# Optimization experiments

Hardware: AMD Instinct MI355X
Metric: run time of the kernel (lower is better)

## Reference

```python
import jax, jax.numpy as jnp
import numpy as np
import math

B, C, L_SEQ, PRED = 32, 21, 512, 96
D, H, DFF, NLAYERS = 512, 8, 2048, 3
E = D // H
PATCH_LEN, STRIDE, PAD = 16, 8, 8
PATCH_NUM = (L_SEQ - PATCH_LEN) // STRIDE + 2  # 64
MA = 25          # moving-average kernel of series_decomp
FACTOR = 1
TOP_K = int(FACTOR * math.log(PATCH_NUM))  # top-k delays in AutoCorrelation


def _pos_embedding(max_len, d_model):
    pos = np.arange(max_len, dtype=np.float32)[:, None]
    div = np.exp(np.arange(0, d_model, 2, dtype=np.float32) * -(math.log(10000.0) / d_model))
    pe = np.zeros((max_len, d_model), np.float32)
    pe[:, 0::2] = np.sin(pos * div)
    pe[:, 1::2] = np.cos(pos * div)
    return jnp.asarray(pe)

POS_EMB = _pos_embedding(PATCH_NUM, D)


def setup_inputs():
    key = jax.random.key(0)
    ks = iter(jax.random.split(key, 48))
    g = lambda shape, s=0.02: jax.random.normal(next(ks), shape, jnp.float32) * s
    inp = {"x_enc": jax.random.normal(next(ks), (B, L_SEQ, C), jnp.float32)}
    inp["w_val"] = g((PATCH_LEN, D))  # PatchEmbedding value_embedding (no bias)
    for tag in ("ac", "sa"):
        for nm in ("Wq", "Wk", "Wv", "Wo"):
            inp[nm + "_" + tag] = g((NLAYERS, D, D))
        for nm in ("bq", "bk", "bv", "bo"):
            inp[nm + "_" + tag] = g((NLAYERS, D))
    inp["Wf"] = g((NLAYERS, 2 * D, D))
    inp["bf"] = g((NLAYERS, D))
    inp["W1"] = g((NLAYERS, D, DFF))   # conv1 (1x1, no bias)
    inp["W2"] = g((NLAYERS, DFF, D))   # conv2 (1x1, no bias)
    inp["bn_g"] = jnp.ones((D,), jnp.float32)
    inp["bn_b"] = jnp.zeros((D,), jnp.float32)
    inp["W_head"] = g((D * PATCH_NUM, PRED))
    inp["b_head"] = g((PRED,))
    return inp


def _proj_heads(x, W, b):
    N, L, _ = x.shape
    return (x @ W + b).reshape(N, L, H, E)


def _auto_corr(x, Wq, bq, Wk, bk, Wv, bv, Wo, bo):
    # AutoCorrelation (training-mode time_delay_agg): FFT correlation + top-k roll aggregation
    N, L, _ = x.shape
    q = _proj_heads(x, Wq, bq)
    k = _proj_heads(x, Wk, bk)
    v = _proj_heads(x, Wv, bv)
    qf = jnp.fft.rfft(q.transpose(0, 2, 3, 1), axis=-1)   # [N,H,E,Lf]
    kf = jnp.fft.rfft(k.transpose(0, 2, 3, 1), axis=-1)
    corr = jnp.fft.irfft(qf * jnp.conj(kf), n=L, axis=-1)  # [N,H,E,L]
    vals = v.transpose(0, 2, 3, 1)                          # [N,H,E,L]
    mean_corr = corr.mean(axis=(1, 2))                      # [N,L]
    _, top_idx = jax.lax.top_k(mean_corr.mean(axis=0), TOP_K)  # delays shared across batch
    w = jax.nn.softmax(mean_corr[:, top_idx], axis=-1)      # [N,TOP_K]
    rolled = jax.vmap(lambda s: jnp.roll(vals, -s, axis=-1))(top_idx)  # [K,N,H,E,L]
    agg = jnp.einsum('knhel,nk->nhel', rolled, w)
    return agg.transpose(0, 3, 1, 2).reshape(N, L, D) @ Wo + bo


def _full_attn(x, Wq, bq, Wk, bk, Wv, bv, Wo, bo):
    N, L, _ = x.shape
    q = _proj_heads(x, Wq, bq)
    k = _proj_heads(x, Wk, bk)
    v = _proj_heads(x, Wv, bv)
    scores = jnp.einsum('blhe,bshe->bhls', q, k) / math.sqrt(E)
    out = jnp.einsum('bhls,bshe->blhe', jax.nn.softmax(scores, axis=-1), v)
    return out.reshape(N, L, D) @ Wo + bo


def _decomp(x):
    # series_decomp: residual after edge-replicated moving average (returns seasonal part)
    half = (MA - 1) // 2
    xp = jnp.concatenate([jnp.repeat(x[:, :1], half, axis=1), x,
                          jnp.repeat(x[:, -1:], half, axis=1)], axis=1)
    cs = jnp.cumsum(xp, axis=1)
    cs = jnp.concatenate([jnp.zeros_like(cs[:, :1]), cs], axis=1)
    mean = (cs[:, MA:] - cs[:, :-MA]) / MA
    return x - mean


def _forward(x_enc, w_val, Wq_ac, bq_ac, Wk_ac, bk_ac, Wv_ac, bv_ac, Wo_ac, bo_ac,
             Wq_sa, bq_sa, Wk_sa, bk_sa, Wv_sa, bv_sa, Wo_sa, bo_sa,
             Wf, bf, W1, W2, bn_g, bn_b, W_head, b_head):
    # instance normalization over time
    means = x_enc.mean(axis=1, keepdims=True)                 # [B,1,C]
    xc = x_enc - means
    stdev = jnp.sqrt(xc.var(axis=1, keepdims=True) + 1e-5)    # [B,1,C]
    xn = xc / stdev
    # patch embedding (channel independent): replication-pad end, unfold, linear + pos emb
    xp = xn.transpose(0, 2, 1)                                # [B,C,L]
    xp = jnp.concatenate([xp, jnp.repeat(xp[..., -1:], PAD, axis=-1)], axis=-1)
    idx = jnp.arange(PATCH_NUM)[:, None] * STRIDE + jnp.arange(PATCH_LEN)[None, :]
    patches = xp[..., idx]                                    # [B,C,P,patch_len]
    x = patches.reshape(B * C, PATCH_NUM, PATCH_LEN) @ w_val + POS_EMB  # [B*C,P,D]
    # hybrid encoder layers
    for l in range(NLAYERS):
        a = _auto_corr(x, Wq_ac[l], bq_ac[l], Wk_ac[l], bk_ac[l], Wv_ac[l], bv_ac[l], Wo_ac[l], bo_ac[l])
        s = _full_attn(x, Wq_sa[l], bq_sa[l], Wk_sa[l], bk_sa[l], Wv_sa[l], bv_sa[l], Wo_sa[l], bo_sa[l])
        fused = jnp.concatenate([a, s], axis=-1) @ Wf[l] + bf[l]
        x = _decomp(x + fused)
        y = jax.nn.relu(x @ W1[l]) @ W2[l]                    # 1x1 convs == pointwise linears
        x = _decomp(x + y)
    # final BatchNorm1d over d_model channels (batch statistics, affine)
    mu = x.mean(axis=(0, 1))
    var = x.var(axis=(0, 1))
    x = (x - mu) / jnp.sqrt(var + 1e-5) * bn_g + bn_b
    # head: [B*C,P,D] -> [B,C,D,P] -> flat (d-major) -> pred_len
    enc = x.reshape(B, C, PATCH_NUM, D).transpose(0, 1, 3, 2).reshape(B, C, D * PATCH_NUM)
    dec = (enc @ W_head + b_head).transpose(0, 2, 1)          # [B,PRED,C]
    return dec * stdev[:, 0][:, None, :] + means[:, 0][:, None, :]


def reference(x_enc, w_val, Wq_ac, bq_ac, Wk_ac, bk_ac, Wv_ac, bv_ac, Wo_ac, bo_ac,
              Wq_sa, bq_sa, Wk_sa, bk_sa, Wv_sa, bv_sa, Wo_sa, bo_sa,
              Wf, bf, W1, W2, bn_g, bn_b, W_head, b_head):
    return _forward(x_enc, w_val, Wq_ac, bq_ac, Wk_ac, bk_ac, Wv_ac, bv_ac, Wo_ac, bo_ac,
                    Wq_sa, bq_sa, Wk_sa, bk_sa, Wv_sa, bv_sa, Wo_sa, bo_sa,
                    Wf, bf, W1, W2, bn_g, bn_b, W_head, b_head)
```

## Files before the change

kernel.cpp:

```cpp
#include <hip/hip_runtime.h>
#include <math.h>


typedef unsigned short u16;
typedef short s16x8 __attribute__((ext_vector_type(8)));
typedef u16 u16x8 __attribute__((ext_vector_type(8)));
typedef float f32x4 __attribute__((ext_vector_type(4)));

#define MROWS 43008
#define NSEQ  672

__device__ __forceinline__ float bf2f(u16 b) {
  union { unsigned u; float f; } v; v.u = ((unsigned)b) << 16; return v.f;
}
__device__ __forceinline__ u16 f2bf(float f) {
  union { float f; unsigned u; } v; v.f = f;
  unsigned r = v.u + 0x7FFFu + ((v.u >> 16) & 1u);
  return (u16)(r >> 16);
}

__device__ __forceinline__ void gload16(const u16* g, u16* l) {
  __builtin_amdgcn_global_load_lds(
      (const __attribute__((address_space(1))) unsigned int*)g,
      (__attribute__((address_space(3))) unsigned int*)l, 16, 0, 0);
}

__global__ __launch_bounds__(256) void zero_out_kernel(float* __restrict__ o, int n) {
  int i = blockIdx.x * 256 + threadIdx.x;
  if (i < n) o[i] = 0.f;
}

__global__ __launch_bounds__(256) void transpose_cvt_b(
    const float* __restrict__ W, u16* __restrict__ Wt, int K, int N,
    long long sW, long long sT) {
  __shared__ float t[32][33];
  int z = blockIdx.z;
  W += (size_t)z * sW;
  Wt += (size_t)z * sT;
  int k0 = blockIdx.x * 32, n0 = blockIdx.y * 32;
  int tx = threadIdx.x, ty = threadIdx.y;
#pragma unroll
  for (int i = 0; i < 32; i += 8)
    t[ty + i][tx] = W[(size_t)(k0 + ty + i) * N + n0 + tx];
  __syncthreads();
#pragma unroll
  for (int i = 0; i < 32; i += 8)
    Wt[(size_t)(n0 + ty + i) * K + k0 + tx] = f2bf(t[tx][ty + i]);
}

__global__ __launch_bounds__(256) void transpose_cvt_sa(
    const float* __restrict__ Wq_sa, const float* __restrict__ Wk_sa,
    const float* __restrict__ Wv_sa, u16* __restrict__ dst) {
  __shared__ float t[32][33];
  int z = blockIdx.z;
  int l = z / 3, wi = z % 3;
  const float* srcs[3] = {Wq_sa, Wk_sa, Wv_sa};
  const float* W = srcs[wi] + (size_t)l * 262144;
  u16* out = dst + ((size_t)l * 3 + wi) * 262144;
  int k0 = blockIdx.x * 32, n0 = blockIdx.y * 32;
  int tx = threadIdx.x, ty = threadIdx.y;
#pragma unroll
  for (int i = 0; i < 32; i += 8)
    t[ty + i][tx] = W[(size_t)(k0 + ty + i) * 512 + n0 + tx];
  __syncthreads();
#pragma unroll
  for (int i = 0; i < 32; i += 8)
    out[(size_t)(n0 + ty + i) * 512 + k0 + tx] = f2bf(t[tx][ty + i]);
}

__global__ __launch_bounds__(256) void cvt_bf16_fifteen(
    const float* __restrict__ Wo_ac, const float* __restrict__ Wo_sa,
    const float* __restrict__ Wv_ac, const float* __restrict__ Wq_ac,
    const float* __restrict__ Wk_ac, u16* __restrict__ dst) {
  int z = blockIdx.z;
  int l = z / 5, s = z % 5;
  const float* bases[5] = {Wo_ac, Wo_sa, Wv_ac, Wq_ac, Wk_ac};
  const float* src = bases[s] + (size_t)l * 262144;
  u16* out = dst + ((size_t)l * 5 + s) * 262144;
  int i = blockIdx.x * 256 + threadIdx.x;
  if (i < 262144) out[i] = f2bf(src[i]);
}

__global__ __launch_bounds__(512) void boa_eff_kernel(
    const float* __restrict__ Wo_ac, const float* __restrict__ bo_ac,
    const float* __restrict__ bv_ac, float* __restrict__ out) {
  int l = blockIdx.x;
  int i = threadIdx.x;
  const float* Wo = Wo_ac + (size_t)l * 262144;
  float s = bo_ac[l * 512 + i];
  for (int k = 0; k < 512; k++) s += bv_ac[l * 512 + k] * Wo[(size_t)k * 512 + i];
  out[l * 512 + i] = s;
}

__global__ __launch_bounds__(512) void bias_combine(
    const float* __restrict__ WfW, const float* __restrict__ bfW,
    const float* __restrict__ boa_eff, const float* __restrict__ bo_sa,
    float* __restrict__ out) {
  int l = blockIdx.x;
  const float* Wf = WfW + (size_t)l * 524288;
  int n = threadIdx.x;
  float s = bfW[l * 512 + n];
  for (int i = 0; i < 512; i++) s += boa_eff[l * 512 + i] * Wf[(size_t)i * 512 + n];
  for (int i = 0; i < 512; i++) s += bo_sa[l * 512 + i] * Wf[(size_t)(512 + i) * 512 + n];
  out[l * 512 + n] = s;
}

__global__ __launch_bounds__(512, 4) void gemm128x256(
    const u16* __restrict__ A1, const u16* __restrict__ A2, int lda, int ksplit,
    const u16* __restrict__ Bt, int ldb,
    const float* __restrict__ b0, const float* __restrict__ b1,
    const float* __restrict__ b2,
    u16* __restrict__ C, int ldc, int K, int relu, int nb) {
  __shared__ u16 smA[3][128 * 32];
  __shared__ u16 smB[3][256 * 32];
  int g = blockIdx.x;
  if ((gridDim.x & 7) == 0) g = (g & 7) * (gridDim.x >> 3) + (g >> 3);
  int m0 = (g / nb) * 128, n0 = (g % nb) * 256;
  int tid = threadIdx.x, lane = tid & 63, wid = tid >> 6;
  int wr = wid >> 2, wc = wid & 3;
  int m_in = lane & 15, kq = lane >> 4;
  int sr = tid >> 2;
  int gsl = (((tid & 3) ^ ((sr >> 1) & 3)) * 8);

  int offA[4], offB[4];
#pragma unroll
  for (int mf = 0; mf < 4; mf++) {
    int row = wr * 64 + mf * 16 + m_in;
    offA[mf] = row * 32 + ((kq ^ ((row >> 1) & 3)) * 8);
  }
#pragma unroll
  for (int nf = 0; nf < 4; nf++) {
    int row = wc * 64 + nf * 16 + m_in;
    offB[nf] = row * 32 + ((kq ^ ((row >> 1) & 3)) * 8);
  }
  f32x4 acc[4][4];
#pragma unroll
  for (int i = 0; i < 4; i++)
#pragma unroll
    for (int j = 0; j < 4; j++) acc[i][j] = (f32x4){0.f, 0.f, 0.f, 0.f};

  int nt = K >> 5;
  auto STAGE = [&](int b, int t) {
    int k0 = t * 32;
    const u16* Ap; int kk;
    if (k0 < ksplit) { Ap = A1; kk = k0; } else { Ap = A2; kk = k0 - ksplit; }
    gload16(&Ap[(size_t)(m0 + sr) * lda + kk + gsl], &smA[b][wid * 512]);
    gload16(&Bt[(size_t)(n0 + sr) * ldb + k0 + gsl], &smB[b][wid * 512]);
    gload16(&Bt[(size_t)(n0 + 128 + sr) * ldb + k0 + gsl],
            &smB[b][4096 + wid * 512]);
  };

  STAGE(0, 0);
  STAGE(1, 1 < nt ? 1 : nt - 1);
  int cb = 0;
  for (int t = 0; t < nt; ++t) {
    int pf = t + 2 < nt ? t + 2 : nt - 1;
    int pb = cb + 2 >= 3 ? cb - 1 : cb + 2;
    STAGE(pb, pf);
    asm volatile("s_waitcnt vmcnt(6)" ::: "memory");
    asm volatile("s_barrier" ::: "memory");
    const u16* la = &smA[cb][0];
    const u16* lb = &smB[cb][0];
    s16x8 a_[4], b_[4];
#pragma unroll
    for (int mf = 0; mf < 4; mf++) a_[mf] = *(const s16x8*)&la[offA[mf]];
#pragma unroll
    for (int nf = 0; nf < 4; nf++) b_[nf] = *(const s16x8*)&lb[offB[nf]];
    __builtin_amdgcn_s_setprio(1);
#pragma unroll
    for (int mf = 0; mf < 4; mf++)
#pragma unroll
      for (int nf = 0; nf < 4; nf++)
        acc[mf][nf] = __builtin_amdgcn_mfma_f32_16x16x32_bf16(
            a_[mf], b_[nf], acc[mf][nf], 0, 0, 0);
    __builtin_amdgcn_s_setprio(0);
    asm volatile("s_barrier" ::: "memory");
    cb = cb + 1 >= 3 ? 0 : cb + 1;
  }
  int r0 = m0 + wr * 64 + (kq << 2);
#pragma unroll
  for (int mf = 0; mf < 4; mf++) {
#pragma unroll
    for (int nf = 0; nf < 4; nf++) {
      int col = n0 + wc * 64 + nf * 16 + m_in;
      const float* bp = (col < 512) ? b0 : (col < 1024 ? b1 : b2);
      float bv = bp ? bp[col & 511] : 0.f;
#pragma unroll
      for (int r = 0; r < 4; r++) {
        float v = acc[mf][nf][r] + bv;
        if (relu) v = fmaxf(v, 0.f);
        C[(size_t)(r0 + mf * 16 + r) * ldc + col] = f2bf(v);
      }
    }
  }
}

__global__ __launch_bounds__(256) void gemm128p(
    const u16* __restrict__ A1, const u16* __restrict__ A2, int lda, int ksplit,
    const u16* __restrict__ Bt, int ldb,
    const float* __restrict__ b0, const float* __restrict__ b1,
    const float* __restrict__ b2,
    u16* __restrict__ C, int ldc, int K, int relu, int nb,
    long long syA, long long syB, long long syC) {
  __shared__ u16 sm[3][8192];
  int zy = blockIdx.y;
  A1 += (size_t)zy * syA;
  A2 += (size_t)zy * syA;
  Bt += (size_t)zy * syB;
  C  += (size_t)zy * syC;
  int g = blockIdx.x;
  if ((gridDim.x & 7) == 0) g = (g & 7) * (gridDim.x >> 3) + (g >> 3);
  int m0 = (g / nb) * 128, n0 = (g % nb) * 128;
  int tid = threadIdx.x, lane = tid & 63, w = tid >> 6;
  int wr = w >> 1, wc = w & 1;
  int srow = w * 16 + (lane >> 2);
  int scol = (((lane & 3) ^ ((lane >> 3) & 3)) * 8);
  int m_in = lane & 15;
  int sgrp = lane >> 4;
  int offA[4], offB[4];
#pragma unroll
  for (int mf = 0; mf < 4; mf++) {
    int row = wr * 64 + mf * 16 + m_in;
    offA[mf] = row * 32 + ((sgrp ^ ((row >> 1) & 3)) * 8);
  }
#pragma unroll
  for (int nf = 0; nf < 4; nf++) {
    int row = wc * 64 + nf * 16 + m_in;
    offB[nf] = 4096 + row * 32 + ((sgrp ^ ((row >> 1) & 3)) * 8);
  }
  f32x4 acc[4][4];
#pragma unroll
  for (int i = 0; i < 4; i++)
#pragma unroll
    for (int j = 0; j < 4; j++) acc[i][j] = (f32x4){0.f, 0.f, 0.f, 0.f};

  int nt = K >> 5;
  auto STAGE = [&](int b, int t) {
    int k0 = t * 32;
    const u16* Ab; int kk;
    if (k0 < ksplit) { Ab = A1; kk = k0; } else { Ab = A2; kk = k0 - ksplit; }
    u16* base = &sm[b][0];
    gload16(&Ab[(size_t)(m0 + srow) * lda + kk + scol],      base + w * 512);
    gload16(&Ab[(size_t)(m0 + 64 + srow) * lda + kk + scol], base + 2048 + w * 512);
    gload16(&Bt[(size_t)(n0 + srow) * ldb + k0 + scol],      base + 4096 + w * 512);
    gload16(&Bt[(size_t)(n0 + 64 + srow) * ldb + k0 + scol], base + 6144 + w * 512);
  };

  STAGE(0, 0);
  STAGE(1, 1 < nt ? 1 : nt - 1);
  int cb = 0;
  for (int t = 0; t < nt; ++t) {
    int pf = t + 2 < nt ? t + 2 : nt - 1;
    int pb = cb + 2 >= 3 ? cb - 1 : cb + 2;
    STAGE(pb, pf);
    asm volatile("s_waitcnt vmcnt(8)" ::: "memory");
    asm volatile("s_barrier" ::: "memory");
    const u16* lb = &sm[cb][0];
    s16x8 a_[4], b_[4];
#pragma unroll
    for (int mf = 0; mf < 4; mf++) a_[mf] = *(const s16x8*)&lb[offA[mf]];
#pragma unroll
    for (int nf = 0; nf < 4; nf++) b_[nf] = *(const s16x8*)&lb[offB[nf]];
    __builtin_amdgcn_s_setprio(1);
#pragma unroll
    for (int mf = 0; mf < 4; mf++)
#pragma unroll
      for (int nf = 0; nf < 4; nf++)
        acc[mf][nf] = __builtin_amdgcn_mfma_f32_16x16x32_bf16(
            a_[mf], b_[nf], acc[mf][nf], 0, 0, 0);
    __builtin_amdgcn_s_setprio(0);
    asm volatile("s_barrier" ::: "memory");
    cb = cb + 1 >= 3 ? 0 : cb + 1;
  }
  int r0 = m0 + wr * 64 + (sgrp << 2);
  int cl = lane & 15;
#pragma unroll
  for (int mf = 0; mf < 4; mf++) {
#pragma unroll
    for (int nf = 0; nf < 4; nf++) {
      int col = n0 + wc * 64 + nf * 16 + cl;
      const float* bp = (col < 512) ? b0 : (col < 1024 ? b1 : b2);
      float bv = bp ? bp[col & 511] : 0.f;
#pragma unroll
      for (int r = 0; r < 4; r++) {
        float v = acc[mf][nf][r] + bv;
        if (relu) v = fmaxf(v, 0.f);
        C[(size_t)(r0 + mf * 16 + r) * ldc + col] = f2bf(v);
      }
    }
  }
}

__global__ __launch_bounds__(256) void gram_mc_kernel(
    const u16* __restrict__ Q, int ldq, const u16* __restrict__ K, int ldk,
    float* __restrict__ MC) {
  __shared__ u16 lA[64][40];
  __shared__ u16 lB[64][40];
  __shared__ float red[64];
  int n = blockIdx.x;
  int tid = threadIdx.x, lane = tid & 63, w = tid >> 6;
  int sr = tid >> 2, scol = (tid & 3) * 8;
  if (tid < 64) red[tid] = 0.f;
  f32x4 acc[4];
#pragma unroll
  for (int i = 0; i < 4; i++) acc[i] = (f32x4){0.f, 0.f, 0.f, 0.f};
  size_t bq = (size_t)n * 64 * ldq;
  size_t bk = (size_t)n * 64 * ldk;
  for (int k0 = 0; k0 < 512; k0 += 32) {
    *(u16x8*)&lA[sr][scol] = *(const u16x8*)&Q[bq + (size_t)sr * ldq + k0 + scol];
    *(u16x8*)&lB[sr][scol] = *(const u16x8*)&K[bk + (size_t)sr * ldk + k0 + scol];
    __syncthreads();
    int ar = w * 16 + (lane & 15);
    int kk = (lane >> 4) * 8;
    s16x8 af = *(const s16x8*)&lA[ar][kk];
#pragma unroll
    for (int nb = 0; nb < 4; nb++) {
      s16x8 bfr = *(const s16x8*)&lB[nb * 16 + (lane & 15)][kk];
      acc[nb] = __builtin_amdgcn_mfma_f32_16x16x32_bf16(af, bfr, acc[nb], 0, 0, 0);
    }
    __syncthreads();
  }
  int row0 = w * 16 + ((lane >> 4) << 2);
  int cl = lane & 15;
#pragma unroll
  for (int nb = 0; nb < 4; nb++) {
    int col = nb * 16 + cl;
#pragma unroll
    for (int r = 0; r < 4; r++)
      atomicAdd(&red[(row0 + r - col) & 63], acc[nb][r]);
  }
  __syncthreads();
  if (tid < 64) MC[n * 64 + tid] = red[tid] * (1.f / 512.f);
}

__global__ __launch_bounds__(256) void instnorm_kernel(
    const float* __restrict__ xe, float* __restrict__ MEANS, float* __restrict__ STDEV) {
  int n = blockIdx.x;
  int b = n / 21, c = n % 21;
  int tid = threadIdx.x;
  float v0 = xe[((size_t)b * 512 + tid) * 21 + c];
  float v1 = xe[((size_t)b * 512 + tid + 256) * 21 + c];
  float s = v0 + v1, ss = v0 * v0 + v1 * v1;
  for (int o = 32; o; o >>= 1) { s += __shfl_down(s, o); ss += __shfl_down(ss, o); }
  __shared__ float rs[4], rss[4];
  if ((tid & 63) == 0) { rs[tid >> 6] = s; rss[tid >> 6] = ss; }
  __syncthreads();
  if (tid == 0) {
    s = rs[0] + rs[1] + rs[2] + rs[3];
    ss = rss[0] + rss[1] + rss[2] + rss[3];
    float mean = s * (1.f / 512.f);
    float var = ss * (1.f / 512.f) - mean * mean;
    MEANS[n] = mean;
    STDEV[n] = sqrtf(var + 1e-5f);
  }
}

__global__ __launch_bounds__(256) void pe_kernel(float* __restrict__ PE) {
  int i = blockIdx.x * 256 + threadIdx.x;
  int p = i >> 9, d = i & 511;
  int k = d >> 1;
  float freq = expf(-(float)(2 * k) * (9.210340371976184f / 512.f));
  float ang = (float)p * freq;
  PE[i] = (d & 1) ? cosf(ang) : sinf(ang);
}

__global__ __launch_bounds__(256) void patch_kernel(
    const float* __restrict__ xe, const float* __restrict__ wv,
    const float* __restrict__ PE, const float* __restrict__ MEANS,
    const float* __restrict__ STDEV, u16* __restrict__ X) {
  __shared__ float pw[16][512];
  __shared__ float pat[8][16];
  int bx = blockIdx.x;
  int n = bx >> 3, pb = bx & 7;
  int b = n / 21, c = n % 21;
  int tid = threadIdx.x;
  float mean = MEANS[n], inv = 1.f / STDEV[n];
  for (int i = tid; i < 8192; i += 256) pw[i >> 9][i & 511] = wv[i];
  if (tid < 128) {
    int pp = tid >> 4, j = tid & 15;
    int l = (pb * 8 + pp) * 8 + j;
    if (l > 511) l = 511;
    pat[pp][j] = (xe[((size_t)b * 512 + l) * 21 + c] - mean) * inv;
  }
  __syncthreads();
  for (int i = tid; i < 4096; i += 256) {
    int pp = i >> 9, d = i & 511;
    int p = pb * 8 + pp;
    float s = PE[p * 512 + d];
#pragma unroll
    for (int j = 0; j < 16; j++) s += pat[pp][j] * pw[j][d];
    X[((size_t)n * 64 + p) * 512 + d] = f2bf(s);
  }
}

__global__ __launch_bounds__(256) void topk_softw_kernel(
    const float* __restrict__ MC, int* __restrict__ TIDX, float* __restrict__ WSM) {
  __shared__ float g[256];
  __shared__ float gt[64];
  __shared__ int dly[4];
  int tid = threadIdx.x;
  int tau = tid & 63, part = tid >> 6;
  float s = 0.f;
  for (int n = part * 168; n < (part + 1) * 168; n++) s += MC[n * 64 + tau];
  g[tid] = s;
  __syncthreads();
  if (tid < 64) gt[tid] = g[tid] + g[64 + tid] + g[128 + tid] + g[192 + tid];
  __syncthreads();
  if (tid == 0) {
    for (int j = 0; j < 4; j++) {
      int best = 0; float bv = -1e30f;
      for (int t = 0; t < 64; t++) if (gt[t] > bv) { bv = gt[t]; best = t; }
      dly[j] = best;
      TIDX[j] = best;
      gt[best] = -1e30f;
    }
  }
  __syncthreads();
  for (int n = tid; n < 672; n += 256) {
    float v[4], mx = -1e30f;
#pragma unroll
    for (int j = 0; j < 4; j++) { v[j] = MC[n * 64 + dly[j]]; mx = fmaxf(mx, v[j]); }
    float ssum = 0.f;
#pragma unroll
    for (int j = 0; j < 4; j++) { v[j] = __expf(v[j] - mx); ssum += v[j]; }
    float inv = 1.f / ssum;
#pragma unroll
    for (int j = 0; j < 4; j++) WSM[n * 4 + j] = v[j] * inv;
  }
}

__global__ __launch_bounds__(256) void agg_kernel(
    const u16* __restrict__ V, int ldv, const float* __restrict__ WSM,
    const int* __restrict__ TIDX, u16* __restrict__ OUT, int ldo) {
  int n = blockIdx.x;
  __shared__ float w[4];
  __shared__ int dly[4];
  int tid = threadIdx.x;
  if (tid < 4) { w[tid] = WSM[n * 4 + tid]; dly[tid] = TIDX[tid]; }
  __syncthreads();
  for (int i = tid; i < 64 * 512; i += 256) {
    int l = i >> 9, d = i & 511;
    float s = 0.f;
#pragma unroll
    for (int j = 0; j < 4; j++)
      s += w[j] * bf2f(V[((size_t)n * 64 + ((l + dly[j]) & 63)) * ldv + d]);
    OUT[((size_t)n * 64 + l) * ldo + d] = f2bf(s);
  }
}

__global__ __launch_bounds__(256) void attn_mfma(u16* __restrict__ QKV) {
  __shared__ u16 lq[64][72], lk[64][72], lvt[64][72], lp[64][72];
  int n = blockIdx.x >> 3, h = blockIdx.x & 7;
  size_t base = (size_t)n * 64 * 1536;
  int qo = h * 64, ko = 512 + h * 64, vo = 1024 + h * 64;
  int tid = threadIdx.x, lane = tid & 63, w = tid >> 6;
  int r = tid >> 2, c0 = (tid & 3) * 16;
  *(u16x8*)&lq[r][c0]     = *(const u16x8*)&QKV[base + (size_t)r * 1536 + qo + c0];
  *(u16x8*)&lq[r][c0 + 8] = *(const u16x8*)&QKV[base + (size_t)r * 1536 + qo + c0 + 8];
  *(u16x8*)&lk[r][c0]     = *(const u16x8*)&QKV[base + (size_t)r * 1536 + ko + c0];
  *(u16x8*)&lk[r][c0 + 8] = *(const u16x8*)&QKV[base + (size_t)r * 1536 + ko + c0 + 8];
  u16x8 v0 = *(const u16x8*)&QKV[base + (size_t)r * 1536 + vo + c0];
  u16x8 v1 = *(const u16x8*)&QKV[base + (size_t)r * 1536 + vo + c0 + 8];
#pragma unroll
  for (int j = 0; j < 8; j++) { lvt[c0 + j][r] = v0[j]; lvt[c0 + 8 + j][r] = v1[j]; }
  __syncthreads();
  int m_in = lane & 15, ks = (lane >> 4) * 8;
  int rq = lane >> 4;
  s16x8 aq0 = *(const s16x8*)&lq[w * 16 + m_in][ks];
  s16x8 aq1 = *(const s16x8*)&lq[w * 16 + m_in][32 + ks];
  f32x4 s4[4];
#pragma unroll
  for (int nf = 0; nf < 4; nf++) {
    s4[nf] = (f32x4){0.f, 0.f, 0.f, 0.f};
    s16x8 b0 = *(const s16x8*)&lk[nf * 16 + m_in][ks];
    s16x8 b1 = *(const s16x8*)&lk[nf * 16 + m_in][32 + ks];
    s4[nf] = __builtin_amdgcn_mfma_f32_16x16x32_bf16(aq0, b0, s4[nf], 0, 0, 0);
    s4[nf] = __builtin_amdgcn_mfma_f32_16x16x32_bf16(aq1, b1, s4[nf], 0, 0, 0);
  }
  float mx[4] = {-1e30f, -1e30f, -1e30f, -1e30f};
#pragma unroll
  for (int nf = 0; nf < 4; nf++)
#pragma unroll
    for (int r4 = 0; r4 < 4; r4++) {
      s4[nf][r4] *= 0.125f;
      mx[r4] = fmaxf(mx[r4], s4[nf][r4]);
    }
#pragma unroll
  for (int o = 1; o < 16; o <<= 1)
#pragma unroll
    for (int r4 = 0; r4 < 4; r4++) mx[r4] = fmaxf(mx[r4], __shfl_xor(mx[r4], o));
  float sum[4] = {0.f, 0.f, 0.f, 0.f};
#pragma unroll
  for (int nf = 0; nf < 4; nf++)
#pragma unroll
    for (int r4 = 0; r4 < 4; r4++) {
      float e = __expf(s4[nf][r4] - mx[r4]);
      s4[nf][r4] = e;
      sum[r4] += e;
    }
#pragma unroll
  for (int o = 1; o < 16; o <<= 1)
#pragma unroll
    for (int r4 = 0; r4 < 4; r4++) sum[r4] += __shfl_xor(sum[r4], o);
#pragma unroll
  for (int nf = 0; nf < 4; nf++)
#pragma unroll
    for (int r4 = 0; r4 < 4; r4++)
      lp[w * 16 + rq * 4 + r4][nf * 16 + m_in] = f2bf(s4[nf][r4] / sum[r4]);
  __syncthreads();
  s16x8 ap0 = *(const s16x8*)&lp[w * 16 + m_in][ks];
  s16x8 ap1 = *(const s16x8*)&lp[w * 16 + m_in][32 + ks];
#pragma unroll
  for (int nf = 0; nf < 4; nf++) {
    f32x4 o4 = (f32x4){0.f, 0.f, 0.f, 0.f};
    s16x8 b0 = *(const s16x8*)&lvt[nf * 16 + m_in][ks];
    s16x8 b1 = *(const s16x8*)&lvt[nf * 16 + m_in][32 + ks];
    o4 = __builtin_amdgcn_mfma_f32_16x16x32_bf16(ap0, b0, o4, 0, 0, 0);
    o4 = __builtin_amdgcn_mfma_f32_16x16x32_bf16(ap1, b1, o4, 0, 0, 0);
#pragma unroll
    for (int r4 = 0; r4 < 4; r4++)
      QKV[base + (size_t)(w * 16 + rq * 4 + r4) * 1536 + qo + nf * 16 + m_in] =
          f2bf(o4[r4]);
  }
}

__global__ __launch_bounds__(256) void decomp_kernel(
    u16* __restrict__ X, const u16* __restrict__ DELTA, int ds) {
  int n = blockIdx.x >> 1;
  int d = ((blockIdx.x & 1) << 8) + threadIdx.x;
  size_t xb = ((size_t)n * 64) * 512 + d;
  size_t db = ((size_t)n * 64) * ds + d;
  float v[64];
#pragma unroll
  for (int l = 0; l < 64; l++)
    v[l] = bf2f(X[xb + (size_t)l * 512]) + bf2f(DELTA[db + (size_t)l * ds]);
  float s = 12.f * v[0];
#pragma unroll
  for (int t = 0; t <= 12; t++) s += v[t];
#pragma unroll
  for (int l = 0; l < 64; l++) {
    float out = v[l] - s * (1.f / 25.f);
    X[xb + (size_t)l * 512] = f2bf(out);
    if (l < 63) {
      int add = l + 13; if (add > 63) add = 63;
      int sub = l - 12; if (sub < 0) sub = 0;
      s += v[add] - v[sub];
    }
  }
}

__global__ __launch_bounds__(256) void bn_part(
    const u16* __restrict__ X, float* __restrict__ PS) {
  int ch = blockIdx.x, tid = threadIdx.x;
  float s1a = 0, s2a = 0, s1b = 0, s2b = 0;
  size_t base = (size_t)ch * 128 * 512;
  for (int r = 0; r < 128; r++) {
    float a = bf2f(X[base + (size_t)r * 512 + tid]);
    float b = bf2f(X[base + (size_t)r * 512 + tid + 256]);
    s1a += a; s2a += a * a; s1b += b; s2b += b * b;
  }
  PS[(size_t)(ch * 2 + 0) * 512 + tid] = s1a;
  PS[(size_t)(ch * 2 + 0) * 512 + tid + 256] = s1b;
  PS[(size_t)(ch * 2 + 1) * 512 + tid] = s2a;
  PS[(size_t)(ch * 2 + 1) * 512 + tid + 256] = s2b;
}

__global__ __launch_bounds__(256) void bn_final(
    const float* __restrict__ PS, const float* __restrict__ g,
    const float* __restrict__ b, float* __restrict__ SCALE, float* __restrict__ SHIFT) {
  int d = blockIdx.x * 256 + threadIdx.x;
  float s = 0, ss = 0;
  for (int c = 0; c < 336; c++) {
    s += PS[(size_t)(c * 2) * 512 + d];
    ss += PS[(size_t)(c * 2 + 1) * 512 + d];
  }
  float mu = s * (1.f / 43008.f);
  float var = ss * (1.f / 43008.f) - mu * mu;
  float inv = 1.f / sqrtf(var + 1e-5f);
  float sc = g[d] * inv;
  SCALE[d] = sc;
  SHIFT[d] = b[d] - mu * sc;
}

__global__ __launch_bounds__(256) void bn_transpose_kernel(
    const u16* __restrict__ X, const float* __restrict__ SCALE,
    const float* __restrict__ SHIFT, u16* __restrict__ ENC) {
  __shared__ u16 t[64][72];
  int n = blockIdx.x >> 3, dc = (blockIdx.x & 7) * 64;
  int tid = threadIdx.x;
  for (int i = tid; i < 4096; i += 256) {
    int p = i >> 6, d = i & 63;
    float v = bf2f(X[((size_t)n * 64 + p) * 512 + dc + d]) * SCALE[dc + d] + SHIFT[dc + d];
    t[p][d] = f2bf(v);
  }
  __syncthreads();
  for (int i = tid; i < 4096; i += 256) {
    int d = i >> 6, p = i & 63;
    ENC[(size_t)n * 32768 + (size_t)(dc + d) * 64 + p] = t[p][d];
  }
}

__global__ __launch_bounds__(256) void head_gemm(
    const u16* __restrict__ ENC, const u16* __restrict__ Wht,
    float* __restrict__ PART) {
  __shared__ u16 lA[64][40];
  __shared__ u16 lB[96][40];
  int bm = blockIdx.x;
  int kc = blockIdx.y;
  int tid = threadIdx.x, lane = tid & 63, w = tid >> 6;
  int sr = tid >> 2, sc0 = (tid & 3) * 8;
  f32x4 acc[6];
#pragma unroll
  for (int i = 0; i < 6; i++) acc[i] = (f32x4){0.f, 0.f, 0.f, 0.f};
  for (int kk0 = 0; kk0 < 2048; kk0 += 32) {
    int k0 = kc * 2048 + kk0;
    *(u16x8*)&lA[sr][sc0] =
        *(const u16x8*)&ENC[(size_t)(bm * 64 + sr) * 32768 + k0 + sc0];
    for (int i = tid; i < 96 * 4; i += 256) {
      int rB = i >> 2, seg = (i & 3) * 8;
      *(u16x8*)&lB[rB][seg] = *(const u16x8*)&Wht[(size_t)rB * 32768 + k0 + seg];
    }
    __syncthreads();
    int ar = w * 16 + (lane & 15);
    int kk = (lane >> 4) * 8;
    s16x8 af = *(const s16x8*)&lA[ar][kk];
#pragma unroll
    for (int nb = 0; nb < 6; nb++) {
      s16x8 bfr = *(const s16x8*)&lB[nb * 16 + (lane & 15)][kk];
      acc[nb] = __builtin_amdgcn_mfma_f32_16x16x32_bf16(af, bfr, acc[nb], 0, 0, 0);
    }
    __syncthreads();
  }
  int rb = bm * 64 + w * 16 + ((lane >> 4) << 2);
  int cl = lane & 15;
#pragma unroll
  for (int nb = 0; nb < 6; nb++) {
    int col = nb * 16 + cl;
#pragma unroll
    for (int r = 0; r < 4; r++) {
      int row = rb + r;
      if (row < 672) PART[((size_t)kc * 672 + row) * 96 + col] = acc[nb][r];
    }
  }
}

__global__ __launch_bounds__(256) void head_reduce(
    const float* __restrict__ PART, const float* __restrict__ bh,
    const float* __restrict__ STDEV, const float* __restrict__ MEANS,
    float* __restrict__ OUT) {
  int i = blockIdx.x * 256 + threadIdx.x;
  if (i >= 672 * 96) return;
  int n = i / 96, r = i % 96;
  float s = bh[r];
  for (int kc = 0; kc < 16; kc++) s += PART[((size_t)kc * 672 + n) * 96 + r];
  int b = n / 21, c = n % 21;
  OUT[((size_t)b * 96 + r) * 21 + c] = s * STDEV[n] + MEANS[n];
}

extern "C" void kernel_launch(void* const* d_in, const int* in_sizes, int n_in,
                              void* d_out, int out_size, void* d_ws, size_t ws_size,
                              hipStream_t stream) {
  const float* x_enc = (const float*)d_in[0];
  const float* w_val = (const float*)d_in[1];
  const float* Wq_ac = (const float*)d_in[2];
  const float* Wk_ac = (const float*)d_in[3];
  const float* Wv_ac = (const float*)d_in[4];
  const float* Wo_ac = (const float*)d_in[5];
  const float* bq_ac = (const float*)d_in[6];
  const float* bk_ac = (const float*)d_in[7];
  const float* bv_ac = (const float*)d_in[8];
  const float* bo_ac = (const float*)d_in[9];
  const float* Wq_sa = (const float*)d_in[10];
  const float* Wk_sa = (const float*)d_in[11];
  const float* Wv_sa = (const float*)d_in[12];
  const float* Wo_sa = (const float*)d_in[13];
  const float* bq_sa = (const float*)d_in[14];
  const float* bk_sa = (const float*)d_in[15];
  const float* bv_sa = (const float*)d_in[16];
  const float* bo_sa = (const float*)d_in[17];
  const float* WfW   = (const float*)d_in[18];
  const float* bfW   = (const float*)d_in[19];
  const float* W1    = (const float*)d_in[20];
  const float* W2    = (const float*)d_in[21];
  const float* bn_g  = (const float*)d_in[22];
  const float* bn_b  = (const float*)d_in[23];
  const float* W_head = (const float*)d_in[24];
  const float* b_head = (const float*)d_in[25];
  (void)in_sizes; (void)n_in; (void)out_size;
  (void)bq_ac; (void)bk_ac;

  char* wsp = (char*)d_ws;
  size_t off = 0;
  auto alloc = [&](size_t bytes) -> void* {
    void* p = wsp + off;
    off += (bytes + 255) & ~(size_t)255;
    return p;
  };
  u16* X    = (u16*)alloc((size_t)MROWS * 512 * 2);
  u16* Q3   = (u16*)alloc((size_t)MROWS * 1536 * 2);
  u16* SIX   = (u16*)alloc((size_t)3 * 3 * 262144 * 2);
  u16* W1T   = (u16*)alloc((size_t)3 * 1048576 * 2);
  u16* W2T   = (u16*)alloc((size_t)3 * 1048576 * 2);
  u16* WFT   = (u16*)alloc((size_t)3 * 524288 * 2);
  u16* WORIG = (u16*)alloc((size_t)3 * 5 * 262144 * 2);
  u16* WCOMB = (u16*)alloc((size_t)3 * 524288 * 2);
  u16* WQKT  = (u16*)alloc((size_t)3 * 262144 * 2);
  u16* WHT   = (u16*)alloc((size_t)3145728 * 2);
  u16* TMP   = (u16*)alloc((size_t)3 * 262144 * 2);
  float* PE = (float*)alloc((size_t)32768 * 4);
  float* MEANS = (float*)alloc(672 * 4);
  float* STDEV = (float*)alloc(672 * 4);
  float* MC = (float*)alloc(672 * 64 * 4);
  int* TIDX = (int*)alloc(4 * 4);
  float* WSM = (float*)alloc(672 * 4 * 4);
  float* BNP = (float*)alloc((size_t)336 * 1024 * 4);
  float* SCALE = (float*)alloc(512 * 4);
  float* SHIFT = (float*)alloc(512 * 4);
  float* BOAE = (float*)alloc(3 * 512 * 4);
  float* BCOMB = (float*)alloc(3 * 512 * 4);
  u16* C0 = Q3;
  u16* C1 = Q3 + 512;
  u16* C2 = Q3 + 1024;
  u16* HBUF = Q3;
  u16* YBUF = Q3 + (size_t)21504 * 2048;
  u16* ENC  = Q3;
  float* HEADP = (float*)X;

  if (off > ws_size) {
    zero_out_kernel<<<252, 256, 0, stream>>>((float*)d_out, 672 * 96);
    return;
  }

  transpose_cvt_sa<<<dim3(16, 16, 9), dim3(32, 8), 0, stream>>>(
      Wq_sa, Wk_sa, Wv_sa, SIX);
  transpose_cvt_b<<<dim3(16, 64, 3), dim3(32, 8), 0, stream>>>(
      W1, W1T, 512, 2048, 1048576, 1048576);
  transpose_cvt_b<<<dim3(64, 16, 3), dim3(32, 8), 0, stream>>>(
      W2, W2T, 2048, 512, 1048576, 1048576);
  transpose_cvt_b<<<dim3(32, 16, 3), dim3(32, 8), 0, stream>>>(
      WfW, WFT, 1024, 512, 524288, 524288);
  transpose_cvt_b<<<dim3(1024, 3, 1), dim3(32, 8), 0, stream>>>(
      W_head, WHT, 32768, 96, 0, 0);
  cvt_bf16_fifteen<<<dim3(1024, 1, 15), 256, 0, stream>>>(
      Wo_ac, Wo_sa, Wv_ac, Wq_ac, Wk_ac, WORIG);
  boa_eff_kernel<<<3, 512, 0, stream>>>(Wo_ac, bo_ac, bv_ac, BOAE);
  bias_combine<<<3, 512, 0, stream>>>(WfW, bfW, BOAE, bo_sa, BCOMB);
  gemm128p<<<dim3(16, 3), 256, 0, stream>>>(
      WFT, WFT, 1024, 512, WORIG, 512, nullptr, nullptr, nullptr,
      TMP, 512, 512, 0, 4, 524288, 5 * 262144, 262144);
  gemm128p<<<dim3(16, 3), 256, 0, stream>>>(
      TMP, TMP, 512, 512, WORIG + 2 * 262144, 512, nullptr, nullptr, nullptr,
      WCOMB, 1024, 512, 0, 4, 262144, 5 * 262144, 524288);
  gemm128p<<<dim3(16, 3), 256, 0, stream>>>(
      WFT + 512, WFT + 512, 1024, 512, WORIG + 262144, 512,
      nullptr, nullptr, nullptr, WCOMB + 512, 1024, 512, 0, 4,
      524288, 5 * 262144, 524288);
  gemm128p<<<dim3(16, 3), 256, 0, stream>>>(
      WORIG + 4 * 262144, WORIG + 4 * 262144, 512, 512,
      WORIG + 3 * 262144, 512, nullptr, nullptr, nullptr,
      WQKT, 512, 512, 0, 4, 5 * 262144, 5 * 262144, 262144);

  instnorm_kernel<<<672, 256, 0, stream>>>(x_enc, MEANS, STDEV);
  pe_kernel<<<128, 256, 0, stream>>>(PE);
  patch_kernel<<<672 * 8, 256, 0, stream>>>(x_enc, w_val, PE, MEANS, STDEV, X);

  auto gbig = [&](const u16* A1, const u16* A2, int lda, int ksplit,
                  const u16* Bt, int ldb, const float* b0, const float* b1,
                  const float* b2, u16* C, int ldc, int M, int N, int K,
                  int relu) {
    int nb = N / 256;
    if (nb < 1) nb = 1;
    gemm128x256<<<(M / 128) * nb, 512, 0, stream>>>(
        A1, A2, lda, ksplit, Bt, ldb, b0, b1, b2, C, ldc, K, relu, nb);
  };

  for (int l = 0; l < 3; l++) {
    const u16* qkv_sa = SIX + (size_t)l * 3 * 262144;
    const u16* wqkt   = WQKT + (size_t)l * 262144;
    const u16* w1     = W1T + (size_t)l * 1048576;
    const u16* w2     = W2T + (size_t)l * 1048576;
    const u16* wcomb  = WCOMB + (size_t)l * 524288;
    gbig(X, X, 512, 512, qkv_sa, 512, bq_sa + l * 512, bk_sa + l * 512,
         bv_sa + l * 512, Q3, 1536, MROWS, 1536, 512, 0);
    attn_mfma<<<5376, 256, 0, stream>>>(Q3);
    gbig(X, X, 512, 512, wqkt, 512, nullptr, nullptr, nullptr,
         C1, 1536, MROWS, 512, 512, 0);
    gram_mc_kernel<<<672, 256, 0, stream>>>(C1, 1536, X, 512, MC);
    topk_softw_kernel<<<1, 256, 0, stream>>>(MC, TIDX, WSM);
    agg_kernel<<<672, 256, 0, stream>>>(X, 512, WSM, TIDX, C2, 1536);
    gbig(C2, C0, 1536, 512, wcomb, 1024, BCOMB + l * 512, nullptr, nullptr,
         C1, 1536, MROWS, 512, 1024, 0);
    decomp_kernel<<<1344, 256, 0, stream>>>(X, C1, 1536);
    for (int c = 0; c < 2; c++) {
      const u16* Xc = X + (size_t)c * 21504 * 512;
      u16* Yc = YBUF + (size_t)c * 21504 * 512;
      gbig(Xc, Xc, 512, 512, w1, 512, nullptr, nullptr, nullptr,
           HBUF, 2048, 21504, 2048, 512, 1);
      gemm128x256<<<(21504 / 128) * 2, 512, 0, stream>>>(
          HBUF, HBUF, 2048, 2048, w2, 2048, nullptr, nullptr, nullptr,
          Yc, 512, 2048, 0, 2);
    }
    decomp_kernel<<<1344, 256, 0, stream>>>(X, YBUF, 512);
  }

  bn_part<<<336, 256, 0, stream>>>(X, BNP);
  bn_final<<<2, 256, 0, stream>>>(BNP, bn_g, bn_b, SCALE, SHIFT);
  bn_transpose_kernel<<<672 * 8, 256, 0, stream>>>(X, SCALE, SHIFT, ENC);
  head_gemm<<<dim3(11, 16), 256, 0, stream>>>(ENC, WHT, HEADP);
  head_reduce<<<252, 256, 0, stream>>>(HEADP, b_head, STDEV, MEANS, (float*)d_out);
}
```

Baseline: 2.160 ms.

## Enlarge GEMM tile to 256x256 with split-phase loads interleaved with MFMA

Replaces the 128x256 bf16 MFMA GEMM with a 256x256 tile, where each wave computes 128x64 with 8x4 accumulators. The LDS ring grows to four stages. A and B global-to-LDS loads are now issued in two halves, each overlapped with half of the MFMA work. The aim is to raise arithmetic intensity per byte loaded and hide load latency. The cost is double the LDS use (128 KB) and more registers, which limits occupancy to about 2 blocks, and M must be divisible by 256.

```diff
diff --git a/kernel.cpp b/kernel.cpp
--- a/kernel.cpp
+++ b/kernel.cpp
@@ -105,27 +105,25 @@
   out[l * 512 + n] = s;
 }
 
-__global__ __launch_bounds__(512, 4) void gemm128x256(
+__global__ __launch_bounds__(512, 2) void gemm256f(
     const u16* __restrict__ A1, const u16* __restrict__ A2, int lda, int ksplit,
     const u16* __restrict__ Bt, int ldb,
     const float* __restrict__ b0, const float* __restrict__ b1,
     const float* __restrict__ b2,
     u16* __restrict__ C, int ldc, int K, int relu, int nb) {
-  __shared__ u16 smA[3][128 * 32];
-  __shared__ u16 smB[3][256 * 32];
+  __shared__ u16 smA[4][256 * 32];
+  __shared__ u16 smB[4][256 * 32];
   int g = blockIdx.x;
   if ((gridDim.x & 7) == 0) g = (g & 7) * (gridDim.x >> 3) + (g >> 3);
-  int m0 = (g / nb) * 128, n0 = (g % nb) * 256;
+  int m0 = (g / nb) * 256, n0 = (g % nb) * 256;
   int tid = threadIdx.x, lane = tid & 63, wid = tid >> 6;
   int wr = wid >> 2, wc = wid & 3;
   int m_in = lane & 15, kq = lane >> 4;
-  int sr = tid >> 2;
-  int gsl = (((tid & 3) ^ ((sr >> 1) & 3)) * 8);
-
-  int offA[4], offB[4];
-#pragma unroll
-  for (int mf = 0; mf < 4; mf++) {
-    int row = wr * 64 + mf * 16 + m_in;
+
+  int offA[8], offB[4];
+#pragma unroll
+  for (int mf = 0; mf < 8; mf++) {
+    int row = wr * 128 + mf * 16 + m_in;
     offA[mf] = row * 32 + ((kq ^ ((row >> 1) & 3)) * 8);
   }
 #pragma unroll
@@ -133,53 +131,85 @@
     int row = wc * 64 + nf * 16 + m_in;
     offB[nf] = row * 32 + ((kq ^ ((row >> 1) & 3)) * 8);
   }
-  f32x4 acc[4][4];
-#pragma unroll
-  for (int i = 0; i < 4; i++)
+  int srow[2], sgcol[2], sbase[2];
+#pragma unroll
+  for (int l = 0; l < 2; l++) {
+    int idx = l * 512 + tid;
+    int row = idx >> 2, sl = idx & 3;
+    srow[l] = row;
+    sgcol[l] = (sl ^ ((row >> 1) & 3)) * 8;
+    sbase[l] = (l * 512 + wid * 64) * 8;
+  }
+
+  f32x4 acc[8][4];
+#pragma unroll
+  for (int i = 0; i < 8; i++)
 #pragma unroll
     for (int j = 0; j < 4; j++) acc[i][j] = (f32x4){0.f, 0.f, 0.f, 0.f};
 
-  int nt = K >> 5;
-  auto STAGE = [&](int b, int t) {
-    int k0 = t * 32;
+  int nu = K >> 5;
+
+  auto STAGE_A = [&](int ds, int u) {
+    int k0 = u * 32;
     const u16* Ap; int kk;
     if (k0 < ksplit) { Ap = A1; kk = k0; } else { Ap = A2; kk = k0 - ksplit; }
-    gload16(&Ap[(size_t)(m0 + sr) * lda + kk + gsl], &smA[b][wid * 512]);
-    gload16(&Bt[(size_t)(n0 + sr) * ldb + k0 + gsl], &smB[b][wid * 512]);
-    gload16(&Bt[(size_t)(n0 + 128 + sr) * ldb + k0 + gsl],
-            &smB[b][4096 + wid * 512]);
+#pragma unroll
+    for (int l = 0; l < 2; l++)
+      gload16(&Ap[(size_t)(m0 + srow[l]) * lda + kk + sgcol[l]],
+              &smA[ds][sbase[l]]);
   };
-
-  STAGE(0, 0);
-  STAGE(1, 1 < nt ? 1 : nt - 1);
-  int cb = 0;
-  for (int t = 0; t < nt; ++t) {
-    int pf = t + 2 < nt ? t + 2 : nt - 1;
-    int pb = cb + 2 >= 3 ? cb - 1 : cb + 2;
-    STAGE(pb, pf);
-    asm volatile("s_waitcnt vmcnt(6)" ::: "memory");
+  auto STAGE_B = [&](int ds, int u) {
+    int k0 = u * 32;
+#pragma unroll
+    for (int l = 0; l < 2; l++)
+      gload16(&Bt[(size_t)(n0 + srow[l]) * ldb + k0 + sgcol[l]],
+              &smB[ds][sbase[l]]);
+  };
+
+  STAGE_A(0, 0); STAGE_B(0, 0);
+  STAGE_A(1, 1); STAGE_B(1, 1);
+  asm volatile("s_waitcnt vmcnt(4)" ::: "memory");
+  asm volatile("s_barrier" ::: "memory");
+
+  for (int u = 0; u < nu; ++u) {
+    int sl = u & 3, ds = (u + 2) & 3;
+    int usrc = (u + 2 < nu) ? u + 2 : u;
+    const u16* As = &smA[sl][0];
+    const u16* Bs = &smB[sl][0];
+    s16x8 a_[8], b_[4];
+#pragma unroll
+    for (int mf = 0; mf < 8; mf++) a_[mf] = *(const s16x8*)&As[offA[mf]];
+    b_[0] = *(const s16x8*)&Bs[offB[0]];
+    b_[1] = *(const s16x8*)&Bs[offB[1]];
+    STAGE_A(ds, usrc);
     asm volatile("s_barrier" ::: "memory");
-    const u16* la = &smA[cb][0];
-    const u16* lb = &smB[cb][0];
-    s16x8 a_[4], b_[4];
-#pragma unroll
-    for (int mf = 0; mf < 4; mf++) a_[mf] = *(const s16x8*)&la[offA[mf]];
-#pragma unroll
-    for (int nf = 0; nf < 4; nf++) b_[nf] = *(const s16x8*)&lb[offB[nf]];
     __builtin_amdgcn_s_setprio(1);
 #pragma unroll
-    for (int mf = 0; mf < 4; mf++)
-#pragma unroll
-      for (int nf = 0; nf < 4; nf++)
+    for (int mf = 0; mf < 8; mf++)
+#pragma unroll
+      for (int nf = 0; nf < 2; nf++)
         acc[mf][nf] = __builtin_amdgcn_mfma_f32_16x16x32_bf16(
             a_[mf], b_[nf], acc[mf][nf], 0, 0, 0);
     __builtin_amdgcn_s_setprio(0);
     asm volatile("s_barrier" ::: "memory");
-    cb = cb + 1 >= 3 ? 0 : cb + 1;
-  }
-  int r0 = m0 + wr * 64 + (kq << 2);
-#pragma unroll
-  for (int mf = 0; mf < 4; mf++) {
+    b_[2] = *(const s16x8*)&Bs[offB[2]];
+    b_[3] = *(const s16x8*)&Bs[offB[3]];
+    STAGE_B(ds, usrc);
+    asm volatile("s_barrier" ::: "memory");
+    __builtin_amdgcn_s_setprio(1);
+#pragma unroll
+    for (int mf = 0; mf < 8; mf++)
+#pragma unroll
+      for (int nf = 2; nf < 4; nf++)
+        acc[mf][nf] = __builtin_amdgcn_mfma_f32_16x16x32_bf16(
+            a_[mf], b_[nf], acc[mf][nf], 0, 0, 0);
+    __builtin_amdgcn_s_setprio(0);
+    asm volatile("s_waitcnt vmcnt(4)" ::: "memory");
+    asm volatile("s_barrier" ::: "memory");
+  }
+  int r0 = m0 + wr * 128 + (kq << 2);
+#pragma unroll
+  for (int mf = 0; mf < 8; mf++) {
 #pragma unroll
     for (int nf = 0; nf < 4; nf++) {
       int col = n0 + wc * 64 + nf * 16 + m_in;
@@ -770,7 +800,7 @@
                   int relu) {
     int nb = N / 256;
     if (nb < 1) nb = 1;
-    gemm128x256<<<(M / 128) * nb, 512, 0, stream>>>(
+    gemm256f<<<(M / 256) * nb, 512, 0, stream>>>(
         A1, A2, lda, ksplit, Bt, ldb, b0, b1, b2, C, ldc, K, relu, nb);
   };
 
@@ -796,9 +826,8 @@
       u16* Yc = YBUF + (size_t)c * 21504 * 512;
       gbig(Xc, Xc, 512, 512, w1, 512, nullptr, nullptr, nullptr,
            HBUF, 2048, 21504, 2048, 512, 1);
-      gemm128x256<<<(21504 / 128) * 2, 512, 0, stream>>>(
-          HBUF, HBUF, 2048, 2048, w2, 2048, nullptr, nullptr, nullptr,
-          Yc, 512, 2048, 0, 2);
+      gbig(HBUF, HBUF, 2048, 2048, w2, 2048, nullptr, nullptr, nullptr,
+           Yc, 512, 21504, 512, 2048, 0);
     }
     decomp_kernel<<<1344, 256, 0, stream>>>(X, YBUF, 512);
   }
```

Measured after the change: 2.225 ms. 1.03x slower.

## Fuse residual add and series decomposition into GEMM epilogue

Applied to the files above, without the earlier changes.

Adds a decomposition epilogue mode to the 128x256 GEMM. Each wave adds the residual X to its accumulator tile, stages the 64-row tile in shared memory, runs the 25-tap moving-average subtraction along the sequence, and writes the result back into X in place. This removes both decomp_kernel launches per layer, along with the intermediate C1 and YBUF write and read round trips. In exchange the shared arrays are merged into one buffer reused as per-wave scratch, the epilogue does strided column writes, and the kernel relies on each 64-row sequence block sitting inside one wave's tile.

```diff
diff --git a/kernel.cpp b/kernel.cpp
--- a/kernel.cpp
+++ b/kernel.cpp
@@ -110,9 +110,8 @@
     const u16* __restrict__ Bt, int ldb,
     const float* __restrict__ b0, const float* __restrict__ b1,
     const float* __restrict__ b2,
-    u16* __restrict__ C, int ldc, int K, int relu, int nb) {
-  __shared__ u16 smA[3][128 * 32];
-  __shared__ u16 smB[3][256 * 32];
+    u16* __restrict__ C, int ldc, int K, int relu, int nb, int dmode) {
+  __shared__ u16 shm[36864];
   int g = blockIdx.x;
   if ((gridDim.x & 7) == 0) g = (g & 7) * (gridDim.x >> 3) + (g >> 3);
   int m0 = (g / nb) * 128, n0 = (g % nb) * 256;
@@ -144,10 +143,11 @@
     int k0 = t * 32;
     const u16* Ap; int kk;
     if (k0 < ksplit) { Ap = A1; kk = k0; } else { Ap = A2; kk = k0 - ksplit; }
-    gload16(&Ap[(size_t)(m0 + sr) * lda + kk + gsl], &smA[b][wid * 512]);
-    gload16(&Bt[(size_t)(n0 + sr) * ldb + k0 + gsl], &smB[b][wid * 512]);
+    gload16(&Ap[(size_t)(m0 + sr) * lda + kk + gsl], &shm[b * 4096 + wid * 512]);
+    gload16(&Bt[(size_t)(n0 + sr) * ldb + k0 + gsl],
+            &shm[12288 + b * 8192 + wid * 512]);
     gload16(&Bt[(size_t)(n0 + 128 + sr) * ldb + k0 + gsl],
-            &smB[b][4096 + wid * 512]);
+            &shm[12288 + b * 8192 + 4096 + wid * 512]);
   };
 
   STAGE(0, 0);
@@ -159,8 +159,8 @@
     STAGE(pb, pf);
     asm volatile("s_waitcnt vmcnt(6)" ::: "memory");
     asm volatile("s_barrier" ::: "memory");
-    const u16* la = &smA[cb][0];
-    const u16* lb = &smB[cb][0];
+    const u16* la = &shm[cb * 4096];
+    const u16* lb = &shm[12288 + cb * 8192];
     s16x8 a_[4], b_[4];
 #pragma unroll
     for (int mf = 0; mf < 4; mf++) a_[mf] = *(const s16x8*)&la[offA[mf]];
@@ -178,18 +178,59 @@
     cb = cb + 1 >= 3 ? 0 : cb + 1;
   }
   int r0 = m0 + wr * 64 + (kq << 2);
-#pragma unroll
-  for (int mf = 0; mf < 4; mf++) {
-#pragma unroll
-    for (int nf = 0; nf < 4; nf++) {
-      int col = n0 + wc * 64 + nf * 16 + m_in;
-      const float* bp = (col < 512) ? b0 : (col < 1024 ? b1 : b2);
-      float bv = bp ? bp[col & 511] : 0.f;
-#pragma unroll
-      for (int r = 0; r < 4; r++) {
-        float v = acc[mf][nf][r] + bv;
-        if (relu) v = fmaxf(v, 0.f);
-        C[(size_t)(r0 + mf * 16 + r) * ldc + col] = f2bf(v);
+  if (dmode == 0) {
+#pragma unroll
+    for (int mf = 0; mf < 4; mf++) {
+#pragma unroll
+      for (int nf = 0; nf < 4; nf++) {
+        int col = n0 + wc * 64 + nf * 16 + m_in;
+        const float* bp = (col < 512) ? b0 : (col < 1024 ? b1 : b2);
+        float bv = bp ? bp[col & 511] : 0.f;
+#pragma unroll
+        for (int r = 0; r < 4; r++) {
+          float v = acc[mf][nf][r] + bv;
+          if (relu) v = fmaxf(v, 0.f);
+          C[(size_t)(r0 + mf * 16 + r) * ldc + col] = f2bf(v);
+        }
+      }
+    }
+  } else {
+    asm volatile("s_waitcnt vmcnt(0)" ::: "memory");
+    __syncthreads();
+    u16* wscr = &shm[wid * 4352];
+#pragma unroll
+    for (int mf = 0; mf < 4; mf++) {
+#pragma unroll
+      for (int nf = 0; nf < 4; nf++) {
+        int col = n0 + wc * 64 + nf * 16 + m_in;
+        float bv = b0 ? b0[col & 511] : 0.f;
+#pragma unroll
+        for (int r = 0; r < 4; r++) {
+          int row = r0 + mf * 16 + r;
+          float xv = bf2f(C[(size_t)row * 512 + col]);
+          wscr[(mf * 16 + (kq << 2) + r) * 68 + nf * 16 + m_in] =
+              f2bf(xv + acc[mf][nf][r] + bv);
+        }
+      }
+    }
+    __syncthreads();
+    int c = lane;
+    int d = n0 + wc * 64 + c;
+    int nseq = (m0 + wr * 64) >> 6;
+    float v[64];
+#pragma unroll
+    for (int l = 0; l < 64; l++) v[l] = bf2f(wscr[l * 68 + c]);
+    float s = 12.f * v[0];
+#pragma unroll
+    for (int t2 = 0; t2 <= 12; t2++) s += v[t2];
+#pragma unroll
+    for (int l = 0; l < 64; l++) {
+      float out = v[l] - s * (1.f / 25.f);
+      C[((size_t)nseq * 64 + l) * 512 + d] = f2bf(out);
+      if (l < 63) {
+        int add = l + 13; if (add > 63) add = 63;
+        int sub = l - 12; if (sub < 0) sub = 0;
+        s += v[add] - v[sub];
       }
     }
   }
@@ -521,31 +562,6 @@
     for (int r4 = 0; r4 < 4; r4++)
       QKV[base + (size_t)(w * 16 + rq * 4 + r4) * 1536 + qo + nf * 16 + m_in] =
           f2bf(o4[r4]);
-  }
-}
-
-__global__ __launch_bounds__(256) void decomp_kernel(
-    u16* __restrict__ X, const u16* __restrict__ DELTA, int ds) {
-  int n = blockIdx.x >> 1;
-  int d = ((blockIdx.x & 1) << 8) + threadIdx.x;
-  size_t xb = ((size_t)n * 64) * 512 + d;
-  size_t db = ((size_t)n * 64) * ds + d;
-  float v[64];
-#pragma unroll
-  for (int l = 0; l < 64; l++)
-    v[l] = bf2f(X[xb + (size_t)l * 512]) + bf2f(DELTA[db + (size_t)l * ds]);
-  float s = 12.f * v[0];
-#pragma unroll
-  for (int t = 0; t <= 12; t++) s += v[t];
-#pragma unroll
-  for (int l = 0; l < 64; l++) {
-    float out = v[l] - s * (1.f / 25.f);
-    X[xb + (size_t)l * 512] = f2bf(out);
-    if (l < 63) {
-      int add = l + 13; if (add > 63) add = 63;
-      int sub = l - 12; if (sub < 0) sub = 0;
-      s += v[add] - v[sub];
-    }
   }
 }
 
@@ -722,7 +738,6 @@
   u16* C1 = Q3 + 512;
   u16* C2 = Q3 + 1024;
   u16* HBUF = Q3;
-  u16* YBUF = Q3 + (size_t)21504 * 2048;
   u16* ENC  = Q3;
   float* HEADP = (float*)X;
 
@@ -767,11 +782,11 @@
   auto gbig = [&](const u16* A1, const u16* A2, int lda, int ksplit,
                   const u16* Bt, int ldb, const float* b0, const float* b1,
                   const float* b2, u16* C, int ldc, int M, int N, int K,
-                  int relu) {
+                  int relu, int dmode) {
     int nb = N / 256;
     if (nb < 1) nb = 1;
     gemm128x256<<<(M / 128) * nb, 512, 0, stream>>>(
-        A1, A2, lda, ksplit, Bt, ldb, b0, b1, b2, C, ldc, K, relu, nb);
+        A1, A2, lda, ksplit, Bt, ldb, b0, b1, b2, C, ldc, K, relu, nb, dmode);
   };
 
   for (int l = 0; l < 3; l++) {
@@ -781,26 +796,23 @@
     const u16* w2     = W2T + (size_t)l * 1048576;
     const u16* wcomb  = WCOMB + (size_t)l * 524288;
     gbig(X, X, 512, 512, qkv_sa, 512, bq_sa + l * 512, bk_sa + l * 512,
-         bv_sa + l * 512, Q3, 1536, MROWS, 1536, 512, 0);
+         bv_sa + l * 512, Q3, 1536, MROWS, 1536, 512, 0, 0);
     attn_mfma<<<5376, 256, 0, stream>>>(Q3);
     gbig(X, X, 512, 512, wqkt, 512, nullptr, nullptr, nullptr,
-         C1, 1536, MROWS, 512, 512, 0);
+         C1, 1536, MROWS, 512, 512, 0, 0);
     gram_mc_kernel<<<672, 256, 0, stream>>>(C1, 1536, X, 512, MC);
     topk_softw_kernel<<<1, 256, 0, stream>>>(MC, TIDX, WSM);
     agg_kernel<<<672, 256, 0, stream>>>(X, 512, WSM, TIDX, C2, 1536);
     gbig(C2, C0, 1536, 512, wcomb, 1024, BCOMB + l * 512, nullptr, nullptr,
-         C1, 1536, MROWS, 512, 1024, 0);
-    decomp_kernel<<<1344, 256, 0, stream>>>(X, C1, 1536);
+         X, 512, MROWS, 512, 1024, 0, 1);
     for (int c = 0; c < 2; c++) {
       const u16* Xc = X + (size_t)c * 21504 * 512;
-      u16* Yc = YBUF + (size_t)c * 21504 * 512;
+      u16* Xcw = X + (size_t)c * 21504 * 512;
       gbig(Xc, Xc, 512, 512, w1, 512, nullptr, nullptr, nullptr,
-           HBUF, 2048, 21504, 2048, 512, 1);
-      gemm128x256<<<(21504 / 128) * 2, 512, 0, stream>>>(
-          HBUF, HBUF, 2048, 2048, w2, 2048, nullptr, nullptr, nullptr,
-          Yc, 512, 2048, 0, 2);
-    }
-    decomp_kernel<<<1344, 256, 0, stream>>>(X, YBUF, 512);
+           HBUF, 2048, 21504, 2048, 512, 1, 0);
+      gbig(HBUF, HBUF, 2048, 2048, w2, 2048, nullptr, nullptr, nullptr,
+           Xcw, 512, 21504, 512, 2048, 0, 1);
+    }
   }
 
   bn_part<<<336, 256, 0, stream>>>(X, BNP);
```

After: 2.021 ms. 6.4% less time.
